# Kernel tuning notes

Measured on AMD Instinct MI355X. Metric: run time of the kernel, lower is better.

## Reference

```python
import jax, jax.numpy as jnp
import numpy as np

B, T, C = 32, 4096, 256


def setup_inputs() -> dict:
    key = jax.random.key(0)
    ks = jax.random.split(key, 10)
    s = lambda *sh: 0.05
    return {
        "gru_output": jax.random.normal(ks[0], (B, T, C), jnp.float32),
        "intensity_curves": jax.random.uniform(ks[1], (B, T), jnp.float32),
        "W1": jax.random.normal(ks[2], (C, 128), jnp.float32) * 0.05,
        "b1": jnp.zeros((128,), jnp.float32),
        "W2": jax.random.normal(ks[3], (128, 64), jnp.float32) * 0.05,
        "b2": jnp.zeros((64,), jnp.float32),
        "W3": jax.random.normal(ks[4], (64, 4), jnp.float32) * 0.05,
        "b3": jnp.zeros((4,), jnp.float32),
        "conv_w": jax.random.normal(ks[5], (1, C, 3), jnp.float32) * 0.05,  # OIH
        "conv_b": jnp.zeros((1,), jnp.float32),
    }


def reference(gru_output, intensity_curves, W1, b1, W2, b2, W3, b3, conv_w, conv_b):
    Bb, Tt, Cc = gru_output.shape
    # per-timestep phase classifier MLP + softmax -> (B,T,4)
    h = jax.nn.relu(gru_output @ W1 + b1)
    h = jax.nn.relu(h @ W2 + b2)
    phase_probs = jax.nn.softmax(h @ W3 + b3, axis=-1)
    # transition scores: Conv1d(C->1,k=3,pad=1) + sigmoid -> (B,T)
    x = jnp.transpose(gru_output, (0, 2, 1))  # (B,C,T)
    ts = jax.lax.conv_general_dilated(x, conv_w, (1,), 'SAME',
                                      dimension_numbers=('NCH', 'OIH', 'NCH'))
    transition_scores = jax.nn.sigmoid(ts[:, 0, :] + conv_b[0])  # (B,T)
    # run-length segments: new segment when dominant phase changes or transition>0.7
    dom = jnp.argmax(phase_probs, axis=-1)  # (B,T) int
    change = (dom[:, 1:] != dom[:, :-1]) | (transition_scores[:, 1:] > 0.7)
    change = jnp.concatenate([jnp.zeros((Bb, 1), bool), change], axis=1)
    seg = jnp.cumsum(change.astype(jnp.int32), axis=1)  # (B,T) segment id per step
    gseg = (seg + jnp.arange(Bb, dtype=jnp.int32)[:, None] * Tt).reshape(-1)
    nseg = Bb * Tt
    cnt = jax.ops.segment_sum(jnp.ones((nseg,), jnp.float32)[: gseg.shape[0]] * 0 + 1.0,
                              gseg, num_segments=nseg)
    sum_int = jax.ops.segment_sum(intensity_curves.reshape(-1), gseg, num_segments=nseg)
    conf_t = jnp.take_along_axis(phase_probs, dom[..., None], axis=2)[..., 0]  # (B,T)
    sum_conf = jax.ops.segment_sum(conf_t.reshape(-1), gseg, num_segments=nseg)
    denom = jnp.maximum(cnt, 1.0)
    mean_int = (sum_int / denom)[gseg].reshape(Bb, Tt)   # segment-mean intensity per step
    mean_conf = (sum_conf / denom)[gseg].reshape(Bb, Tt)  # segment-mean confidence per step
    return phase_probs, transition_scores, seg, mean_int, mean_conf
```

## Files before the change

kernel.cpp:

```cpp
#include <hip/hip_runtime.h>

#define B_ 32
#define T_ 4096
#define C_ 256
#define R_ (B_*T_)
#define H1_ 128
#define H2_ 64

#define TB 32

#define PROBS_OFF 0
#define TS_OFF  (R_*4)
#define SEG_OFF (TS_OFF + R_)
#define MI_OFF  (SEG_OFF + R_)
#define MC_OFF  (MI_OFF + R_)

#define XS_OFF  0
#define XS_P    260
#define W1S_OFF 8320
#define H1S_OFF 8320
#define H1S_P   132
#define W2S_OFF 0
#define SMEMF   12544

__device__ __forceinline__ void fma4(float4& a, float s, const float4& b) {
  a.x = fmaf(s, b.x, a.x); a.y = fmaf(s, b.y, a.y);
  a.z = fmaf(s, b.z, a.z); a.w = fmaf(s, b.w, a.w);
}

__global__ __launch_bounds__(256, 4) void mlp_conv_kernel(
    const float* __restrict__ X, const float* __restrict__ W1, const float* __restrict__ b1,
    const float* __restrict__ W2, const float* __restrict__ b2,
    const float* __restrict__ W3, const float* __restrict__ b3,
    const float* __restrict__ CW, const float* __restrict__ CB,
    float* __restrict__ out)
{
  __shared__ float sm[SMEMF];
  const int tid  = threadIdx.x;
  const int row0 = blockIdx.x * TB;

  float4 st0 = *(const float4*)&W1[0 * 1024 + tid * 4];
  float4 st1 = *(const float4*)&W1[1 * 1024 + tid * 4];
  float4 st2 = *(const float4*)&W1[2 * 1024 + tid * 4];
  float4 st3 = *(const float4*)&W1[3 * 1024 + tid * 4];

  #pragma unroll
  for (int i2 = 0; i2 < 8; ++i2) {
    int g = tid + 256 * i2;
    int r = g >> 6, m = g & 63;
    float4 v = *(const float4*)&X[(size_t)(row0 + r) * C_ + m * 4];
    *(float4*)&sm[XS_OFF + r * XS_P + m * 4] = v;
  }
  __syncthreads();

  {
    const int l = tid & 63, w = tid >> 6;
    const int rowi = w * 8 + (l & 7);
    const int p = l >> 3;
    const int grow = row0 + rowi;
    const int tb = grow & (T_ - 1);
    float s = 0.f;
    #pragma unroll
    for (int cc = 0; cc < 8; ++cc) {
      const int c = p * 32 + cc * 4;
      float4 x0 = *(const float4*)&sm[XS_OFF + rowi * XS_P + c];
      float4 xm, xp;
      if (tb == 0)             xm = make_float4(0.f, 0.f, 0.f, 0.f);
      else if (rowi >= 1)      xm = *(const float4*)&sm[XS_OFF + (rowi - 1) * XS_P + c];
      else                     xm = *(const float4*)&X[(size_t)(grow - 1) * C_ + c];
      if (tb == T_ - 1)        xp = make_float4(0.f, 0.f, 0.f, 0.f);
      else if (rowi + 1 < TB)  xp = *(const float4*)&sm[XS_OFF + (rowi + 1) * XS_P + c];
      else                     xp = *(const float4*)&X[(size_t)(grow + 1) * C_ + c];
      float4 wa = *(const float4*)&CW[c * 3 + 0];
      float4 wb = *(const float4*)&CW[c * 3 + 4];
      float4 wc = *(const float4*)&CW[c * 3 + 8];
      s += xm.x * wa.x + x0.x * wa.y + xp.x * wa.z;
      s += xm.y * wa.w + x0.y * wb.x + xp.y * wb.y;
      s += xm.z * wb.z + x0.z * wb.w + xp.z * wc.x;
      s += xm.w * wc.y + x0.w * wc.z + xp.w * wc.w;
    }
    s += __shfl_xor(s, 8);
    s += __shfl_xor(s, 16);
    s += __shfl_xor(s, 32);
    if (p == 0) out[TS_OFF + grow] = 1.f / (1.f + expf(-(s + CB[0])));
  }

  const int rt = tid >> 5, ct = tid & 31;
  const int rb = rt * 4;
  float4 acc0 = make_float4(0.f, 0.f, 0.f, 0.f);
  float4 acc1 = acc0, acc2 = acc0, acc3 = acc0;
  for (int kc = 0; kc < 8; ++kc) {
    *(float4*)&sm[W1S_OFF + 0 * 1024 + tid * 4] = st0;
    *(float4*)&sm[W1S_OFF + 1 * 1024 + tid * 4] = st1;
    *(float4*)&sm[W1S_OFF + 2 * 1024 + tid * 4] = st2;
    *(float4*)&sm[W1S_OFF + 3 * 1024 + tid * 4] = st3;
    __syncthreads();
    if (kc + 1 < 8) {
      const float* wp = W1 + (size_t)(kc + 1) * 4096;
      st0 = *(const float4*)&wp[0 * 1024 + tid * 4];
      st1 = *(const float4*)&wp[1 * 1024 + tid * 4];
      st2 = *(const float4*)&wp[2 * 1024 + tid * 4];
      st3 = *(const float4*)&wp[3 * 1024 + tid * 4];
    } else {
      st0 = ((const float4*)W2)[tid +   0];
      st1 = ((const float4*)W2)[tid + 256];
      st2 = ((const float4*)W2)[tid + 512];
      st3 = ((const float4*)W2)[tid + 768];
    }
    #pragma unroll
    for (int k4 = 0; k4 < 8; ++k4) {
      const int kb = kc * 32 + k4 * 4;
      float4 a0 = *(const float4*)&sm[XS_OFF + (rb + 0) * XS_P + kb];
      float4 a1 = *(const float4*)&sm[XS_OFF + (rb + 1) * XS_P + kb];
      float4 a2 = *(const float4*)&sm[XS_OFF + (rb + 2) * XS_P + kb];
      float4 a3 = *(const float4*)&sm[XS_OFF + (rb + 3) * XS_P + kb];
      float4 q0 = *(const float4*)&sm[W1S_OFF + (k4 * 4 + 0) * H1_ + ct * 4];
      float4 q1 = *(const float4*)&sm[W1S_OFF + (k4 * 4 + 1) * H1_ + ct * 4];
      float4 q2 = *(const float4*)&sm[W1S_OFF + (k4 * 4 + 2) * H1_ + ct * 4];
      float4 q3 = *(const float4*)&sm[W1S_OFF + (k4 * 4 + 3) * H1_ + ct * 4];
      fma4(acc0, a0.x, q0); fma4(acc0, a0.y, q1); fma4(acc0, a0.z, q2); fma4(acc0, a0.w, q3);
      fma4(acc1, a1.x, q0); fma4(acc1, a1.y, q1); fma4(acc1, a1.z, q2); fma4(acc1, a1.w, q3);
      fma4(acc2, a2.x, q0); fma4(acc2, a2.y, q1); fma4(acc2, a2.z, q2); fma4(acc2, a2.w, q3);
      fma4(acc3, a3.x, q0); fma4(acc3, a3.y, q1); fma4(acc3, a3.z, q2); fma4(acc3, a3.w, q3);
    }
    __syncthreads();
  }

  const int ct2 = tid & 15;
  float4 t4a = ((const float4*)W2)[tid + 1024];
  float4 t4b = ((const float4*)W2)[tid + 1280];
  float4 t4c = ((const float4*)W2)[tid + 1536];
  float4 t4d = ((const float4*)W2)[tid + 1792];
  float4 w30 = ((const float4*)W3)[ct2 * 4 + 0];
  float4 w31 = ((const float4*)W3)[ct2 * 4 + 1];
  float4 w32 = ((const float4*)W3)[ct2 * 4 + 2];
  float4 w33 = ((const float4*)W3)[ct2 * 4 + 3];
  float4 b3v = *(const float4*)&b3[0];
  {
    float4 bb = *(const float4*)&b1[ct * 4];
    float4 h;
    h = acc0; h.x = fmaxf(h.x + bb.x, 0.f); h.y = fmaxf(h.y + bb.y, 0.f);
              h.z = fmaxf(h.z + bb.z, 0.f); h.w = fmaxf(h.w + bb.w, 0.f);
    *(float4*)&sm[H1S_OFF + (rb + 0) * H1S_P + ct * 4] = h;
    h = acc1; h.x = fmaxf(h.x + bb.x, 0.f); h.y = fmaxf(h.y + bb.y, 0.f);
              h.z = fmaxf(h.z + bb.z, 0.f); h.w = fmaxf(h.w + bb.w, 0.f);
    *(float4*)&sm[H1S_OFF + (rb + 1) * H1S_P + ct * 4] = h;
    h = acc2; h.x = fmaxf(h.x + bb.x, 0.f); h.y = fmaxf(h.y + bb.y, 0.f);
              h.z = fmaxf(h.z + bb.z, 0.f); h.w = fmaxf(h.w + bb.w, 0.f);
    *(float4*)&sm[H1S_OFF + (rb + 2) * H1S_P + ct * 4] = h;
    h = acc3; h.x = fmaxf(h.x + bb.x, 0.f); h.y = fmaxf(h.y + bb.y, 0.f);
              h.z = fmaxf(h.z + bb.z, 0.f); h.w = fmaxf(h.w + bb.w, 0.f);
    *(float4*)&sm[H1S_OFF + (rb + 3) * H1S_P + ct * 4] = h;
  }
  *(float4*)&sm[W2S_OFF + (tid +    0) * 4] = st0;
  *(float4*)&sm[W2S_OFF + (tid +  256) * 4] = st1;
  *(float4*)&sm[W2S_OFF + (tid +  512) * 4] = st2;
  *(float4*)&sm[W2S_OFF + (tid +  768) * 4] = st3;
  *(float4*)&sm[W2S_OFF + (tid + 1024) * 4] = t4a;
  *(float4*)&sm[W2S_OFF + (tid + 1280) * 4] = t4b;
  *(float4*)&sm[W2S_OFF + (tid + 1536) * 4] = t4c;
  *(float4*)&sm[W2S_OFF + (tid + 1792) * 4] = t4d;
  __syncthreads();

  const int rt2 = tid >> 4;
  float4 c0 = make_float4(0.f, 0.f, 0.f, 0.f), c1 = c0;
  #pragma unroll 8
  for (int k4 = 0; k4 < 32; ++k4) {
    float4 a0 = *(const float4*)&sm[H1S_OFF + (rt2 * 2 + 0) * H1S_P + k4 * 4];
    float4 a1 = *(const float4*)&sm[H1S_OFF + (rt2 * 2 + 1) * H1S_P + k4 * 4];
    float4 q0 = *(const float4*)&sm[W2S_OFF + (k4 * 4 + 0) * H2_ + ct2 * 4];
    float4 q1 = *(const float4*)&sm[W2S_OFF + (k4 * 4 + 1) * H2_ + ct2 * 4];
    float4 q2 = *(const float4*)&sm[W2S_OFF + (k4 * 4 + 2) * H2_ + ct2 * 4];
    float4 q3 = *(const float4*)&sm[W2S_OFF + (k4 * 4 + 3) * H2_ + ct2 * 4];
    fma4(c0, a0.x, q0); fma4(c0, a0.y, q1); fma4(c0, a0.z, q2); fma4(c0, a0.w, q3);
    fma4(c1, a1.x, q0); fma4(c1, a1.y, q1); fma4(c1, a1.z, q2); fma4(c1, a1.w, q3);
  }
  {
    float4 bb = *(const float4*)&b2[ct2 * 4];
    c0.x = fmaxf(c0.x + bb.x, 0.f); c0.y = fmaxf(c0.y + bb.y, 0.f);
    c0.z = fmaxf(c0.z + bb.z, 0.f); c0.w = fmaxf(c0.w + bb.w, 0.f);
    c1.x = fmaxf(c1.x + bb.x, 0.f); c1.y = fmaxf(c1.y + bb.y, 0.f);
    c1.z = fmaxf(c1.z + bb.z, 0.f); c1.w = fmaxf(c1.w + bb.w, 0.f);
  }

  float4 L0 = make_float4(0.f, 0.f, 0.f, 0.f), L1 = L0;
  fma4(L0, c0.x, w30); fma4(L0, c0.y, w31); fma4(L0, c0.z, w32); fma4(L0, c0.w, w33);
  fma4(L1, c1.x, w30); fma4(L1, c1.y, w31); fma4(L1, c1.z, w32); fma4(L1, c1.w, w33);
  #pragma unroll
  for (int d = 1; d < 16; d <<= 1) {
    L0.x += __shfl_xor(L0.x, d); L0.y += __shfl_xor(L0.y, d);
    L0.z += __shfl_xor(L0.z, d); L0.w += __shfl_xor(L0.w, d);
    L1.x += __shfl_xor(L1.x, d); L1.y += __shfl_xor(L1.y, d);
    L1.z += __shfl_xor(L1.z, d); L1.w += __shfl_xor(L1.w, d);
  }
  {
    float4 L = (ct2 < 8) ? L0 : L1;
    const int grow = row0 + rt2 * 2 + ((ct2 < 8) ? 0 : 1);
    L.x += b3v.x; L.y += b3v.y; L.z += b3v.z; L.w += b3v.w;
    float mx = fmaxf(fmaxf(L.x, L.y), fmaxf(L.z, L.w));
    float e0 = expf(L.x - mx), e1 = expf(L.y - mx), e2 = expf(L.z - mx), e3 = expf(L.w - mx);
    float inv = 1.f / ((e0 + e1) + (e2 + e3));
    float p0 = e0 * inv, p1 = e1 * inv, p2 = e2 * inv, p3 = e3 * inv;
    if ((ct2 & 7) == 0) {
      *(float4*)&out[PROBS_OFF + (size_t)grow * 4] = make_float4(p0, p1, p2, p3);
      int dom = 0; float pm = p0;
      if (p1 > pm) { pm = p1; dom = 1; }
      if (p2 > pm) { pm = p2; dom = 2; }
      if (p3 > pm) { pm = p3; dom = 3; }
      out[MI_OFF + grow] = (float)dom;
      out[MC_OFF + grow] = pm;
    }
  }
}

__global__ __launch_bounds__(1024, 1) void seg_kernel(
    const float* __restrict__ inten, float* __restrict__ out)
{
  __shared__ float scnt[T_], ssi[T_], ssc[T_];
  __shared__ int wtot[16], wexcl[16];
  const int tid = threadIdx.x;
  const int lane = tid & 63, wid = tid >> 6;
  const size_t base = (size_t)blockIdx.x * T_;
  const float* tsS = out + TS_OFF;
  float* segO = out + SEG_OFF;
  float* miO  = out + MI_OFF;
  float* mcO  = out + MC_OFF;
  const int t4 = tid * 4;

  float4 dv = *(const float4*)&miO[base + t4];
  float4 tv = *(const float4*)&tsS[base + t4];
  float4 iv = *(const float4*)&inten[base + t4];
  float4 cv = *(const float4*)&mcO[base + t4];
  float pd = (tid == 0) ? 0.f : miO[base + t4 - 1];

  for (int i = tid; i < T_; i += 1024) { scnt[i] = 0.f; ssi[i] = 0.f; ssc[i] = 0.f; }

  int c0 = (t4 == 0) ? 0 : (((dv.x != pd)   || (tv.x > 0.7f)) ? 1 : 0);
  int c1 = ((dv.y != dv.x) || (tv.y > 0.7f)) ? 1 : 0;
  int c2 = ((dv.z != dv.y) || (tv.z > 0.7f)) ? 1 : 0;
  int c3 = ((dv.w != dv.z) || (tv.w > 0.7f)) ? 1 : 0;
  int l0 = c0, l1 = c0 + c1, l2 = l1 + c2, l3 = l2 + c3;
  const int tsum = l3;

  int v = tsum;
  #pragma unroll
  for (int d = 1; d < 64; d <<= 1) {
    int o = __shfl_up(v, (unsigned)d);
    if (lane >= d) v += o;
  }
  if (lane == 63) wtot[wid] = v;
  __syncthreads();
  if (tid < 16) {
    int x = wtot[tid];
    int xx = x;
    #pragma unroll
    for (int d = 1; d < 16; d <<= 1) {
      int o = __shfl_up(xx, (unsigned)d);
      if (tid >= d) xx += o;
    }
    wexcl[tid] = xx - x;
  }
  __syncthreads();
  const int texcl = wexcl[wid] + (v - tsum);
  const int s0 = texcl + l0, s1 = texcl + l1, s2 = texcl + l2, s3 = texcl + l3;

  {
    int cur = s0; float aI = iv.x, aC = cv.x, aN = 1.f;
    if (s1 == cur) { aI += iv.y; aC += cv.y; aN += 1.f; }
    else { atomicAdd(&ssi[cur], aI); atomicAdd(&ssc[cur], aC); atomicAdd(&scnt[cur], aN);
           cur = s1; aI = iv.y; aC = cv.y; aN = 1.f; }
    if (s2 == cur) { aI += iv.z; aC += cv.z; aN += 1.f; }
    else { atomicAdd(&ssi[cur], aI); atomicAdd(&ssc[cur], aC); atomicAdd(&scnt[cur], aN);
           cur = s2; aI = iv.z; aC = cv.z; aN = 1.f; }
    if (s3 == cur) { aI += iv.w; aC += cv.w; aN += 1.f; }
    else { atomicAdd(&ssi[cur], aI); atomicAdd(&ssc[cur], aC); atomicAdd(&scnt[cur], aN);
           cur = s3; aI = iv.w; aC = cv.w; aN = 1.f; }
    atomicAdd(&ssi[cur], aI); atomicAdd(&ssc[cur], aC); atomicAdd(&scnt[cur], aN);
  }
  __syncthreads();

  float n0 = scnt[s0], n1 = scnt[s1], n2 = scnt[s2], n3 = scnt[s3];
  float4 m4, q4, g4;
  m4.x = ssi[s0] / n0; m4.y = ssi[s1] / n1; m4.z = ssi[s2] / n2; m4.w = ssi[s3] / n3;
  q4.x = ssc[s0] / n0; q4.y = ssc[s1] / n1; q4.z = ssc[s2] / n2; q4.w = ssc[s3] / n3;
  g4.x = (float)s0; g4.y = (float)s1; g4.z = (float)s2; g4.w = (float)s3;
  *(float4*)&segO[base + t4] = g4;
  *(float4*)&miO[base + t4]  = m4;
  *(float4*)&mcO[base + t4]  = q4;
}

extern "C" void kernel_launch(void* const* d_in, const int* in_sizes, int n_in,
                              void* d_out, int out_size, void* d_ws, size_t ws_size,
                              hipStream_t stream) {
  (void)in_sizes; (void)n_in; (void)out_size; (void)d_ws; (void)ws_size;
  const float* X   = (const float*)d_in[0];
  const float* INT = (const float*)d_in[1];
  const float* W1  = (const float*)d_in[2];
  const float* B1  = (const float*)d_in[3];
  const float* W2  = (const float*)d_in[4];
  const float* B2  = (const float*)d_in[5];
  const float* W3  = (const float*)d_in[6];
  const float* B3  = (const float*)d_in[7];
  const float* CW  = (const float*)d_in[8];
  const float* CB  = (const float*)d_in[9];
  float* out = (float*)d_out;

  hipLaunchKernelGGL(mlp_conv_kernel, dim3(R_ / TB), dim3(256), 0, stream,
                     X, W1, B1, W2, B2, W3, B3, CW, CB, out);
  hipLaunchKernelGGL(seg_kernel, dim3(B_), dim3(1024), 0, stream, INT, out);
}
```

Baseline: 206.5 us.

## Double row tile to 64 with 8x4 register blocking in MLP kernel

```diff
diff --git a/kernel.cpp b/kernel.cpp
--- a/kernel.cpp
+++ b/kernel.cpp
@@ -7,7 +7,7 @@
 #define H1_ 128
 #define H2_ 64
 
-#define TB 32
+#define TB 64
 
 #define PROBS_OFF 0
 #define TS_OFF  (R_*4)
@@ -16,19 +16,19 @@
 #define MC_OFF  (MI_OFF + R_)
 
 #define XS_OFF  0
-#define XS_P    260
-#define W1S_OFF 8320
-#define H1S_OFF 8320
+#define XS_P    268
+#define H1S_OFF 0
 #define H1S_P   132
-#define W2S_OFF 0
-#define SMEMF   12544
+#define W2S_OFF 8448
+#define W1S_OFF 17152
+#define SMEMF   19200
 
 __device__ __forceinline__ void fma4(float4& a, float s, const float4& b) {
   a.x = fmaf(s, b.x, a.x); a.y = fmaf(s, b.y, a.y);
   a.z = fmaf(s, b.z, a.z); a.w = fmaf(s, b.w, a.w);
 }
 
-__global__ __launch_bounds__(256, 4) void mlp_conv_kernel(
+__global__ __launch_bounds__(256, 2) void mlp_conv_kernel(
     const float* __restrict__ X, const float* __restrict__ W1, const float* __restrict__ b1,
     const float* __restrict__ W2, const float* __restrict__ b2,
     const float* __restrict__ W3, const float* __restrict__ b3,
@@ -37,15 +37,15 @@
 {
   __shared__ float sm[SMEMF];
   const int tid  = threadIdx.x;
+  const int l    = tid & 63;
+  const int w    = tid >> 6;
   const int row0 = blockIdx.x * TB;
 
-  float4 st0 = *(const float4*)&W1[0 * 1024 + tid * 4];
-  float4 st1 = *(const float4*)&W1[1 * 1024 + tid * 4];
-  float4 st2 = *(const float4*)&W1[2 * 1024 + tid * 4];
-  float4 st3 = *(const float4*)&W1[3 * 1024 + tid * 4];
-
-  #pragma unroll
-  for (int i2 = 0; i2 < 8; ++i2) {
+  float4 st0 = ((const float4*)W1)[tid];
+  float4 st1 = ((const float4*)W1)[tid + 256];
+
+  #pragma unroll
+  for (int i2 = 0; i2 < 16; ++i2) {
     int g = tid + 256 * i2;
     int r = g >> 6, m = g & 63;
     float4 v = *(const float4*)&X[(size_t)(row0 + r) * C_ + m * 4];
@@ -53,9 +53,9 @@
   }
   __syncthreads();
 
-  {
-    const int l = tid & 63, w = tid >> 6;
-    const int rowi = w * 8 + (l & 7);
+  #pragma unroll
+  for (int half = 0; half < 2; ++half) {
+    const int rowi = half * 32 + w * 8 + (l & 7);
     const int p = l >> 3;
     const int grow = row0 + rowi;
     const int tb = grow & (T_ - 1);
@@ -86,130 +86,135 @@
   }
 
   const int rt = tid >> 5, ct = tid & 31;
-  const int rb = rt * 4;
-  float4 acc0 = make_float4(0.f, 0.f, 0.f, 0.f);
-  float4 acc1 = acc0, acc2 = acc0, acc3 = acc0;
-  for (int kc = 0; kc < 8; ++kc) {
-    *(float4*)&sm[W1S_OFF + 0 * 1024 + tid * 4] = st0;
-    *(float4*)&sm[W1S_OFF + 1 * 1024 + tid * 4] = st1;
-    *(float4*)&sm[W1S_OFF + 2 * 1024 + tid * 4] = st2;
-    *(float4*)&sm[W1S_OFF + 3 * 1024 + tid * 4] = st3;
+  const int rb = rt * 8;
+  float4 acc[8];
+  #pragma unroll
+  for (int r = 0; r < 8; ++r) acc[r] = make_float4(0.f, 0.f, 0.f, 0.f);
+
+  for (int kc = 0; kc < 16; ++kc) {
+    *(float4*)&sm[W1S_OFF + tid * 4]         = st0;
+    *(float4*)&sm[W1S_OFF + (tid + 256) * 4] = st1;
     __syncthreads();
-    if (kc + 1 < 8) {
-      const float* wp = W1 + (size_t)(kc + 1) * 4096;
-      st0 = *(const float4*)&wp[0 * 1024 + tid * 4];
-      st1 = *(const float4*)&wp[1 * 1024 + tid * 4];
-      st2 = *(const float4*)&wp[2 * 1024 + tid * 4];
-      st3 = *(const float4*)&wp[3 * 1024 + tid * 4];
+    if (kc + 1 < 16) {
+      const float* wp = W1 + (size_t)(kc + 1) * 2048;
+      st0 = ((const float4*)wp)[tid];
+      st1 = ((const float4*)wp)[tid + 256];
     } else {
-      st0 = ((const float4*)W2)[tid +   0];
+      st0 = ((const float4*)W2)[tid];
       st1 = ((const float4*)W2)[tid + 256];
-      st2 = ((const float4*)W2)[tid + 512];
-      st3 = ((const float4*)W2)[tid + 768];
-    }
-    #pragma unroll
-    for (int k4 = 0; k4 < 8; ++k4) {
-      const int kb = kc * 32 + k4 * 4;
+    }
+    #pragma unroll
+    for (int k4 = 0; k4 < 4; ++k4) {
+      const int kb = kc * 16 + k4 * 4;
       float4 a0 = *(const float4*)&sm[XS_OFF + (rb + 0) * XS_P + kb];
       float4 a1 = *(const float4*)&sm[XS_OFF + (rb + 1) * XS_P + kb];
       float4 a2 = *(const float4*)&sm[XS_OFF + (rb + 2) * XS_P + kb];
       float4 a3 = *(const float4*)&sm[XS_OFF + (rb + 3) * XS_P + kb];
+      float4 a4 = *(const float4*)&sm[XS_OFF + (rb + 4) * XS_P + kb];
+      float4 a5 = *(const float4*)&sm[XS_OFF + (rb + 5) * XS_P + kb];
+      float4 a6 = *(const float4*)&sm[XS_OFF + (rb + 6) * XS_P + kb];
+      float4 a7 = *(const float4*)&sm[XS_OFF + (rb + 7) * XS_P + kb];
       float4 q0 = *(const float4*)&sm[W1S_OFF + (k4 * 4 + 0) * H1_ + ct * 4];
       float4 q1 = *(const float4*)&sm[W1S_OFF + (k4 * 4 + 1) * H1_ + ct * 4];
       float4 q2 = *(const float4*)&sm[W1S_OFF + (k4 * 4 + 2) * H1_ + ct * 4];
       float4 q3 = *(const float4*)&sm[W1S_OFF + (k4 * 4 + 3) * H1_ + ct * 4];
-      fma4(acc0, a0.x, q0); fma4(acc0, a0.y, q1); fma4(acc0, a0.z, q2); fma4(acc0, a0.w, q3);
-      fma4(acc1, a1.x, q0); fma4(acc1, a1.y, q1); fma4(acc1, a1.z, q2); fma4(acc1, a1.w, q3);
-      fma4(acc2, a2.x, q0); fma4(acc2, a2.y, q1); fma4(acc2, a2.z, q2); fma4(acc2, a2.w, q3);
-      fma4(acc3, a3.x, q0); fma4(acc3, a3.y, q1); fma4(acc3, a3.z, q2); fma4(acc3, a3.w, q3);
+      fma4(acc[0], a0.x, q0); fma4(acc[0], a0.y, q1); fma4(acc[0], a0.z, q2); fma4(acc[0], a0.w, q3);
+      fma4(acc[1], a1.x, q0); fma4(acc[1], a1.y, q1); fma4(acc[1], a1.z, q2); fma4(acc[1], a1.w, q3);
+      fma4(acc[2], a2.x, q0); fma4(acc[2], a2.y, q1); fma4(acc[2], a2.z, q2); fma4(acc[2], a2.w, q3);
+      fma4(acc[3], a3.x, q0); fma4(acc[3], a3.y, q1); fma4(acc[3], a3.z, q2); fma4(acc[3], a3.w, q3);
+      fma4(acc[4], a4.x, q0); fma4(acc[4], a4.y, q1); fma4(acc[4], a4.z, q2); fma4(acc[4], a4.w, q3);
+      fma4(acc[5], a5.x, q0); fma4(acc[5], a5.y, q1); fma4(acc[5], a5.z, q2); fma4(acc[5], a5.w, q3);
+      fma4(acc[6], a6.x, q0); fma4(acc[6], a6.y, q1); fma4(acc[6], a6.z, q2); fma4(acc[6], a6.w, q3);
+      fma4(acc[7], a7.x, q0); fma4(acc[7], a7.y, q1); fma4(acc[7], a7.z, q2); fma4(acc[7], a7.w, q3);
     }
     __syncthreads();
   }
 
-  const int ct2 = tid & 15;
-  float4 t4a = ((const float4*)W2)[tid + 1024];
-  float4 t4b = ((const float4*)W2)[tid + 1280];
-  float4 t4c = ((const float4*)W2)[tid + 1536];
-  float4 t4d = ((const float4*)W2)[tid + 1792];
+  const int rt2 = tid >> 4, ct2 = tid & 15;
+  float4 w2r[6];
+  #pragma unroll
+  for (int i = 0; i < 6; ++i) w2r[i] = ((const float4*)W2)[tid + 512 + 256 * i];
   float4 w30 = ((const float4*)W3)[ct2 * 4 + 0];
   float4 w31 = ((const float4*)W3)[ct2 * 4 + 1];
   float4 w32 = ((const float4*)W3)[ct2 * 4 + 2];
   float4 w33 = ((const float4*)W3)[ct2 * 4 + 3];
   float4 b3v = *(const float4*)&b3[0];
+
   {
-    float4 bb = *(const float4*)&b1[ct * 4];
-    float4 h;
-    h = acc0; h.x = fmaxf(h.x + bb.x, 0.f); h.y = fmaxf(h.y + bb.y, 0.f);
-              h.z = fmaxf(h.z + bb.z, 0.f); h.w = fmaxf(h.w + bb.w, 0.f);
-    *(float4*)&sm[H1S_OFF + (rb + 0) * H1S_P + ct * 4] = h;
-    h = acc1; h.x = fmaxf(h.x + bb.x, 0.f); h.y = fmaxf(h.y + bb.y, 0.f);
-              h.z = fmaxf(h.z + bb.z, 0.f); h.w = fmaxf(h.w + bb.w, 0.f);
-    *(float4*)&sm[H1S_OFF + (rb + 1) * H1S_P + ct * 4] = h;
-    h = acc2; h.x = fmaxf(h.x + bb.x, 0.f); h.y = fmaxf(h.y + bb.y, 0.f);
-              h.z = fmaxf(h.z + bb.z, 0.f); h.w = fmaxf(h.w + bb.w, 0.f);
-    *(float4*)&sm[H1S_OFF + (rb + 2) * H1S_P + ct * 4] = h;
-    h = acc3; h.x = fmaxf(h.x + bb.x, 0.f); h.y = fmaxf(h.y + bb.y, 0.f);
-              h.z = fmaxf(h.z + bb.z, 0.f); h.w = fmaxf(h.w + bb.w, 0.f);
-    *(float4*)&sm[H1S_OFF + (rb + 3) * H1S_P + ct * 4] = h;
-  }
-  *(float4*)&sm[W2S_OFF + (tid +    0) * 4] = st0;
-  *(float4*)&sm[W2S_OFF + (tid +  256) * 4] = st1;
-  *(float4*)&sm[W2S_OFF + (tid +  512) * 4] = st2;
-  *(float4*)&sm[W2S_OFF + (tid +  768) * 4] = st3;
-  *(float4*)&sm[W2S_OFF + (tid + 1024) * 4] = t4a;
-  *(float4*)&sm[W2S_OFF + (tid + 1280) * 4] = t4b;
-  *(float4*)&sm[W2S_OFF + (tid + 1536) * 4] = t4c;
-  *(float4*)&sm[W2S_OFF + (tid + 1792) * 4] = t4d;
-  __syncthreads();
-
-  const int rt2 = tid >> 4;
-  float4 c0 = make_float4(0.f, 0.f, 0.f, 0.f), c1 = c0;
-  #pragma unroll 8
+    float4 bb = ((const float4*)b1)[ct];
+    #pragma unroll
+    for (int r = 0; r < 8; ++r) {
+      float4 h = acc[r];
+      h.x = fmaxf(h.x + bb.x, 0.f); h.y = fmaxf(h.y + bb.y, 0.f);
+      h.z = fmaxf(h.z + bb.z, 0.f); h.w = fmaxf(h.w + bb.w, 0.f);
+      *(float4*)&sm[H1S_OFF + (rb + r) * H1S_P + ct * 4] = h;
+    }
+  }
+  *(float4*)&sm[W2S_OFF + tid * 4]         = st0;
+  *(float4*)&sm[W2S_OFF + (tid + 256) * 4] = st1;
+  #pragma unroll
+  for (int i = 0; i < 6; ++i)
+    *(float4*)&sm[W2S_OFF + (tid + 512 + 256 * i) * 4] = w2r[i];
+  __syncthreads();
+
+  float4 acc2[4];
+  #pragma unroll
+  for (int j = 0; j < 4; ++j) acc2[j] = make_float4(0.f, 0.f, 0.f, 0.f);
+  #pragma unroll 4
   for (int k4 = 0; k4 < 32; ++k4) {
-    float4 a0 = *(const float4*)&sm[H1S_OFF + (rt2 * 2 + 0) * H1S_P + k4 * 4];
-    float4 a1 = *(const float4*)&sm[H1S_OFF + (rt2 * 2 + 1) * H1S_P + k4 * 4];
+    float4 a0 = *(const float4*)&sm[H1S_OFF + (rt2 * 4 + 0) * H1S_P + k4 * 4];
+    float4 a1 = *(const float4*)&sm[H1S_OFF + (rt2 * 4 + 1) * H1S_P + k4 * 4];
+    float4 a2 = *(const float4*)&sm[H1S_OFF + (rt2 * 4 + 2) * H1S_P + k4 * 4];
+    float4 a3 = *(const float4*)&sm[H1S_OFF + (rt2 * 4 + 3) * H1S_P + k4 * 4];
     float4 q0 = *(const float4*)&sm[W2S_OFF + (k4 * 4 + 0) * H2_ + ct2 * 4];
     float4 q1 = *(const float4*)&sm[W2S_OFF + (k4 * 4 + 1) * H2_ + ct2 * 4];
     float4 q2 = *(const float4*)&sm[W2S_OFF + (k4 * 4 + 2) * H2_ + ct2 * 4];
     float4 q3 = *(const float4*)&sm[W2S_OFF + (k4 * 4 + 3) * H2_ + ct2 * 4];
-    fma4(c0, a0.x, q0); fma4(c0, a0.y, q1); fma4(c0, a0.z, q2); fma4(c0, a0.w, q3);
-    fma4(c1, a1.x, q0); fma4(c1, a1.y, q1); fma4(c1, a1.z, q2); fma4(c1, a1.w, q3);
-  }
+    fma4(acc2[0], a0.x, q0); fma4(acc2[0], a0.y, q1); fma4(acc2[0], a0.z, q2); fma4(acc2[0], a0.w, q3);
+    fma4(acc2[1], a1.x, q0); fma4(acc2[1], a1.y, q1); fma4(acc2[1], a1.z, q2); fma4(acc2[1], a1.w, q3);
+    fma4(acc2[2], a2.x, q0); fma4(acc2[2], a2.y, q1); fma4(acc2[2], a2.z, q2); fma4(acc2[2], a2.w, q3);
+    fma4(acc2[3], a3.x, q0); fma4(acc2[3], a3.y, q1); fma4(acc2[3], a3.z, q2); fma4(acc2[3], a3.w, q3);
+  }
+
+  float4 L[4];
   {
-    float4 bb = *(const float4*)&b2[ct2 * 4];
-    c0.x = fmaxf(c0.x + bb.x, 0.f); c0.y = fmaxf(c0.y + bb.y, 0.f);
-    c0.z = fmaxf(c0.z + bb.z, 0.f); c0.w = fmaxf(c0.w + bb.w, 0.f);
-    c1.x = fmaxf(c1.x + bb.x, 0.f); c1.y = fmaxf(c1.y + bb.y, 0.f);
-    c1.z = fmaxf(c1.z + bb.z, 0.f); c1.w = fmaxf(c1.w + bb.w, 0.f);
-  }
-
-  float4 L0 = make_float4(0.f, 0.f, 0.f, 0.f), L1 = L0;
-  fma4(L0, c0.x, w30); fma4(L0, c0.y, w31); fma4(L0, c0.z, w32); fma4(L0, c0.w, w33);
-  fma4(L1, c1.x, w30); fma4(L1, c1.y, w31); fma4(L1, c1.z, w32); fma4(L1, c1.w, w33);
+    float4 bb = ((const float4*)b2)[ct2];
+    #pragma unroll
+    for (int r = 0; r < 4; ++r) {
+      float4 h = acc2[r];
+      h.x = fmaxf(h.x + bb.x, 0.f); h.y = fmaxf(h.y + bb.y, 0.f);
+      h.z = fmaxf(h.z + bb.z, 0.f); h.w = fmaxf(h.w + bb.w, 0.f);
+      float4 t = make_float4(0.f, 0.f, 0.f, 0.f);
+      fma4(t, h.x, w30); fma4(t, h.y, w31); fma4(t, h.z, w32); fma4(t, h.w, w33);
+      L[r] = t;
+    }
+  }
   #pragma unroll
   for (int d = 1; d < 16; d <<= 1) {
-    L0.x += __shfl_xor(L0.x, d); L0.y += __shfl_xor(L0.y, d);
-    L0.z += __shfl_xor(L0.z, d); L0.w += __shfl_xor(L0.w, d);
-    L1.x += __shfl_xor(L1.x, d); L1.y += __shfl_xor(L1.y, d);
-    L1.z += __shfl_xor(L1.z, d); L1.w += __shfl_xor(L1.w, d);
-  }
-  {
-    float4 L = (ct2 < 8) ? L0 : L1;
-    const int grow = row0 + rt2 * 2 + ((ct2 < 8) ? 0 : 1);
-    L.x += b3v.x; L.y += b3v.y; L.z += b3v.z; L.w += b3v.w;
-    float mx = fmaxf(fmaxf(L.x, L.y), fmaxf(L.z, L.w));
-    float e0 = expf(L.x - mx), e1 = expf(L.y - mx), e2 = expf(L.z - mx), e3 = expf(L.w - mx);
+    #pragma unroll
+    for (int r = 0; r < 4; ++r) {
+      L[r].x += __shfl_xor(L[r].x, d);
+      L[r].y += __shfl_xor(L[r].y, d);
+      L[r].z += __shfl_xor(L[r].z, d);
+      L[r].w += __shfl_xor(L[r].w, d);
+    }
+  }
+
+  if (ct2 < 4) {
+    float4 Lv = L[ct2];
+    const int grow = row0 + rt2 * 4 + ct2;
+    Lv.x += b3v.x; Lv.y += b3v.y; Lv.z += b3v.z; Lv.w += b3v.w;
+    float mx = fmaxf(fmaxf(Lv.x, Lv.y), fmaxf(Lv.z, Lv.w));
+    float e0 = expf(Lv.x - mx), e1 = expf(Lv.y - mx), e2 = expf(Lv.z - mx), e3 = expf(Lv.w - mx);
     float inv = 1.f / ((e0 + e1) + (e2 + e3));
     float p0 = e0 * inv, p1 = e1 * inv, p2 = e2 * inv, p3 = e3 * inv;
-    if ((ct2 & 7) == 0) {
-      *(float4*)&out[PROBS_OFF + (size_t)grow * 4] = make_float4(p0, p1, p2, p3);
-      int dom = 0; float pm = p0;
-      if (p1 > pm) { pm = p1; dom = 1; }
-      if (p2 > pm) { pm = p2; dom = 2; }
-      if (p3 > pm) { pm = p3; dom = 3; }
-      out[MI_OFF + grow] = (float)dom;
-      out[MC_OFF + grow] = pm;
-    }
+    *(float4*)&out[PROBS_OFF + (size_t)grow * 4] = make_float4(p0, p1, p2, p3);
+    int dom = 0; float pm = p0;
+    if (p1 > pm) { pm = p1; dom = 1; }
+    if (p2 > pm) { pm = p2; dom = 2; }
+    if (p3 > pm) { pm = p3; dom = 3; }
+    out[MI_OFF + grow] = (float)dom;
+    out[MC_OFF + grow] = pm;
   }
 }
 
```

New measurement: 179.5 us, median of 2. -13.0%, faster.
